# Kernel tuning notes

Hardware: AMD Instinct MI355X
Metric: run time of the kernel (lower is better)

Reference implementation:

```python
import jax, jax.numpy as jnp
import numpy as np
from jax import lax

D_MODEL = 1024
D_INNER = 2048   # expand * d_model
D_STATE = 16
DT_RANK = 128    # ceil(d_inner / 16)
K = 4            # depthwise conv kernel size
EPS = 1e-5


def setup_inputs() -> dict:
    key = jax.random.key(0)
    ks = jax.random.split(key, 12)
    x = jax.random.normal(ks[0], (2, 1024, D_MODEL), dtype=jnp.float32)
    norm_w = jnp.ones((D_MODEL,), jnp.float32)
    norm_b = jnp.zeros((D_MODEL,), jnp.float32)
    # linear weights stored (in, out)
    in_proj_w = jax.random.normal(ks[1], (D_MODEL, 2 * D_INNER), jnp.float32) * (D_MODEL ** -0.5)
    conv_w = jax.random.normal(ks[2], (D_INNER, K), jnp.float32) * (K ** -0.5)
    conv_b = jnp.zeros((D_INNER,), jnp.float32)
    x_proj_w = jax.random.normal(ks[3], (D_INNER, DT_RANK + 2 * D_STATE), jnp.float32) * (D_INNER ** -0.5)
    dt_init_std = DT_RANK ** -0.5
    dt_proj_w = jax.random.uniform(ks[4], (DT_RANK, D_INNER), jnp.float32, -dt_init_std, dt_init_std)
    dt = jnp.exp(jax.random.uniform(ks[5], (D_INNER,), jnp.float32)
                 * (np.log(0.1) - np.log(0.001)) + np.log(0.001))
    dt_proj_b = dt + jnp.log(-jnp.expm1(-dt))  # inverse-softplus init
    A_log = jax.random.normal(ks[6], (D_INNER, D_STATE), jnp.float32)
    D_param = jax.random.normal(ks[7], (D_INNER,), jnp.float32)
    out_proj_w = jax.random.normal(ks[8], (D_INNER, D_MODEL), jnp.float32) * (D_INNER ** -0.5)
    return dict(x=x, norm_w=norm_w, norm_b=norm_b, in_proj_w=in_proj_w,
                conv_w=conv_w, conv_b=conv_b, x_proj_w=x_proj_w,
                dt_proj_w=dt_proj_w, dt_proj_b=dt_proj_b, A_log=A_log,
                D_param=D_param, out_proj_w=out_proj_w)


def _layer_norm(x, w, b):
    mu = jnp.mean(x, axis=-1, keepdims=True)
    var = jnp.mean(jnp.square(x - mu), axis=-1, keepdims=True)
    return (x - mu) * lax.rsqrt(var + EPS) * w + b


def _causal_depthwise_conv(x, w, b):
    # x: (B, L, D); w: (D, K). Equivalent to torch conv1d(pad=3)[:, :, :L].
    L = x.shape[1]
    xp = jnp.pad(x, ((0, 0), (K - 1, 0), (0, 0)))
    out = b
    for k in range(K):
        out = out + w[:, k] * xp[:, k:k + L, :]
    return out


def _selective_scan(u, delta, A, B, C, D):
    # u, delta: (B, L, D); A: (D, N); B, C: (B, L, N); D: (D,)
    deltaA = jnp.exp(jnp.einsum('bld,dn->bldn', delta, A))           # (B,L,D,N)
    deltaBu = jnp.einsum('bld,bln,bld->bldn', delta, B, u)           # (B,L,D,N)
    bsz, _, d, n = deltaA.shape

    def step(h, inp):
        dA, dBu, Ct = inp
        h = dA * h + dBu                                             # (B,D,N)
        y = jnp.einsum('bdn,bn->bd', h, Ct)
        return h, y

    h0 = jnp.zeros((bsz, d, n), u.dtype)
    _, ys = lax.scan(step, h0,
                     (deltaA.transpose(1, 0, 2, 3),
                      deltaBu.transpose(1, 0, 2, 3),
                      C.transpose(1, 0, 2)))
    y = ys.transpose(1, 0, 2)                                        # (B,L,D)
    return y + u * D


def reference(x, norm_w, norm_b, in_proj_w, conv_w, conv_b, x_proj_w,
              dt_proj_w, dt_proj_b, A_log, D_param, out_proj_w):
    residual = x
    h = _layer_norm(x, norm_w, norm_b)
    xr = h @ in_proj_w                                               # (B,L,2*D_inner)
    xs, res = xr[..., :D_INNER], xr[..., D_INNER:]
    xs = _causal_depthwise_conv(xs, conv_w, conv_b)
    xs = jax.nn.silu(xs)
    # S6
    A = -jnp.exp(A_log)
    xp = xs @ x_proj_w                                               # (B,L,dt_rank+2N)
    dr = xp[..., :DT_RANK]
    Bm = xp[..., DT_RANK:DT_RANK + D_STATE]
    Cm = xp[..., DT_RANK + D_STATE:]
    delta = jax.nn.softplus(dr @ dt_proj_w + dt_proj_b)
    y = _selective_scan(xs, delta, A, Bm, Cm, D_param)
    y = y * jax.nn.silu(res)
    return y @ out_proj_w + residual
```

## Files before the change

### kernel.cpp

```cpp
#include <hip/hip_runtime.h>
#include <hip/hip_bf16.h>
#include <math.h>

#define BSZ     2
#define LLEN    1024
#define DM      1024
#define DI      2048
#define DS      16
#define DTR     128
#define NXP     160
#define MROWS   (BSZ*LLEN)
#define NCH     32
#define CHL     (LLEN/NCH)

typedef short  bf16x8 __attribute__((ext_vector_type(8)));
typedef float  f32x4  __attribute__((ext_vector_type(4)));

__device__ __forceinline__ unsigned short f2bf(float f) {
    unsigned int u = __float_as_uint(f);
    return (unsigned short)((u + 0x7FFFu + ((u >> 16) & 1u)) >> 16);
}

__global__ __launch_bounds__(256) void ln_bf16(
    const float* __restrict__ x, const float* __restrict__ w,
    const float* __restrict__ b, unsigned short* __restrict__ hb)
{
    const int r = blockIdx.x;
    const int tid = threadIdx.x;
    const float4 v = ((const float4*)(x + (size_t)r * DM))[tid];
    float s  = v.x + v.y + v.z + v.w;
    float q  = v.x*v.x + v.y*v.y + v.z*v.z + v.w*v.w;
    #pragma unroll
    for (int o = 32; o > 0; o >>= 1) {
        s += __shfl_down(s, o);
        q += __shfl_down(q, o);
    }
    __shared__ float ss[4], sq[4];
    if ((tid & 63) == 0) { ss[tid >> 6] = s; sq[tid >> 6] = q; }
    __syncthreads();
    s = ss[0] + ss[1] + ss[2] + ss[3];
    q = sq[0] + sq[1] + sq[2] + sq[3];
    const float mu  = s * (1.0f / DM);
    const float var = q * (1.0f / DM) - mu * mu;
    const float rs  = rsqrtf(var + 1e-5f);
    const float4 wv = ((const float4*)w)[tid];
    const float4 bv = ((const float4*)b)[tid];
    ushort4 ob;
    ob.x = f2bf((v.x - mu) * rs * wv.x + bv.x);
    ob.y = f2bf((v.y - mu) * rs * wv.y + bv.y);
    ob.z = f2bf((v.z - mu) * rs * wv.z + bv.z);
    ob.w = f2bf((v.w - mu) * rs * wv.w + bv.w);
    *(ushort4*)&hb[(size_t)r * DM + (tid << 2)] = ob;
}

__global__ __launch_bounds__(256) void cast_transpose3(
    const float* __restrict__ s0, unsigned short* __restrict__ d0_,
    const float* __restrict__ s1, unsigned short* __restrict__ d1_,
    const float* __restrict__ s2, unsigned short* __restrict__ d2_)
{
    const int bid = blockIdx.x;
    const float* src; unsigned short* dst; int K, N, bx, by;
    if (bid < 1024)      { src = s0; dst = d0_; K = 1024; N = 4096;
                           bx = bid & 63; by = bid >> 6; }
    else if (bid < 1120) { int lb = bid - 1024; src = s1; dst = d1_;
                           K = 2048; N = 160; bx = lb % 3; by = lb / 3; }
    else                 { int lb = bid - 1120; src = s2; dst = d2_;
                           K = 128; N = 2048; bx = lb & 31; by = lb >> 5; }
    __shared__ unsigned short t[64][68];
    const int tid = threadIdx.x;
    const int k0 = by * 64, n0 = bx * 64;
    #pragma unroll
    for (int q = 0; q < 4; ++q) {
        int idx = q * 256 + tid;
        int r = idx >> 4, c = (idx & 15) * 4;
        if (k0 + r < K) {
            #pragma unroll
            for (int e = 0; e < 4; ++e)
                if (n0 + c + e < N)
                    t[r][c + e] = f2bf(src[(size_t)(k0 + r) * N + n0 + c + e]);
        }
    }
    __syncthreads();
    #pragma unroll
    for (int q = 0; q < 4; ++q) {
        int idx = q * 256 + tid;
        int r = idx >> 4, c = (idx & 15) * 4;
        if (n0 + r < N) {
            #pragma unroll
            for (int e = 0; e < 4; ++e)
                if (k0 + c + e < K)
                    dst[(size_t)(n0 + r) * K + k0 + c + e] = t[c + e][r];
        }
    }
}

__global__ __launch_bounds__(256) void cast_transpose_g(
    const float* __restrict__ src, unsigned short* __restrict__ dst,
    int K, int N)
{
    __shared__ unsigned short t[64][68];
    const int tid = threadIdx.x;
    const int k0 = blockIdx.y * 64, n0 = blockIdx.x * 64;
    #pragma unroll
    for (int q = 0; q < 4; ++q) {
        int idx = q * 256 + tid;
        int r = idx >> 4, c = (idx & 15) * 4;
        if (k0 + r < K) {
            #pragma unroll
            for (int e = 0; e < 4; ++e)
                if (n0 + c + e < N)
                    t[r][c + e] = f2bf(src[(size_t)(k0 + r) * N + n0 + c + e]);
        }
    }
    __syncthreads();
    #pragma unroll
    for (int q = 0; q < 4; ++q) {
        int idx = q * 256 + tid;
        int r = idx >> 4, c = (idx & 15) * 4;
        if (n0 + r < N) {
            #pragma unroll
            for (int e = 0; e < 4; ++e)
                if (k0 + c + e < K)
                    dst[(size_t)(n0 + r) * K + k0 + c + e] = t[c + e][r];
        }
    }
}

template<int BM, int BN, int EPI>
__global__ __launch_bounds__(256) void gemm_bf16(
    const unsigned short* __restrict__ A,
    const unsigned short* __restrict__ Bt,
    float* __restrict__ C, int M, int N, int K, int kpb,
    const float* __restrict__ bias,
    const float* __restrict__ resid)
{
    constexpr int LDT = 72;
    __shared__ unsigned short As[BM][LDT];
    __shared__ unsigned short Bs[BN][LDT];
    const int tid  = threadIdx.x;
    const int m0   = blockIdx.y * BM;
    const int n0   = blockIdx.x * BN;
    const int kbeg = blockIdx.z * kpb;
    const int kend = kbeg + kpb;
    float* Cw = C + (size_t)blockIdx.z * M * N;
    const int wave = tid >> 6;
    const int lane = tid & 63;
    const int wr   = (wave >> 1) * (BM / 2);
    const int wc   = (wave & 1) * (BN / 2);
    constexpr int FM = BM / 32;
    constexpr int FN = BN / 32;
    const int l15 = lane & 15;
    const int kg  = lane >> 4;

    f32x4 acc[FM][FN] = {};

    for (int kt = kbeg; kt < kend; kt += 64) {
        __syncthreads();
        #pragma unroll
        for (int q = 0; q < BM / 32; ++q) {
            int idx = q * 256 + tid;
            int r = idx >> 3, c = (idx & 7) * 8;
            *(uint4*)&As[r][c] = *(const uint4*)&A[(size_t)(m0 + r) * K + kt + c];
        }
        #pragma unroll
        for (int q = 0; q < BN / 32; ++q) {
            int idx = q * 256 + tid;
            int r = idx >> 3, c = (idx & 7) * 8;
            *(uint4*)&Bs[r][c] = *(const uint4*)&Bt[(size_t)(n0 + r) * K + kt + c];
        }
        __syncthreads();
        #pragma unroll
        for (int ks = 0; ks < 2; ++ks) {
            bf16x8 af[FM], bfr[FN];
            #pragma unroll
            for (int i = 0; i < FM; ++i)
                af[i] = *(const bf16x8*)&As[wr + i * 16 + l15][ks * 32 + kg * 8];
            #pragma unroll
            for (int j = 0; j < FN; ++j)
                bfr[j] = *(const bf16x8*)&Bs[wc + j * 16 + l15][ks * 32 + kg * 8];
            #pragma unroll
            for (int i = 0; i < FM; ++i)
                #pragma unroll
                for (int j = 0; j < FN; ++j)
                    acc[i][j] = __builtin_amdgcn_mfma_f32_16x16x32_bf16(
                        af[i], bfr[j], acc[i][j], 0, 0, 0);
        }
    }
    #pragma unroll
    for (int i = 0; i < FM; ++i) {
        #pragma unroll
        for (int j = 0; j < FN; ++j) {
            const int row = m0 + wr + i * 16 + kg * 4;
            const int col = n0 + wc + j * 16 + l15;
            #pragma unroll
            for (int r = 0; r < 4; ++r) {
                float v = acc[i][j][r];
                if (EPI == 1) {
                    float t = v + bias[col];
                    v = (t > 20.f) ? t : log1pf(__expf(t));
                } else if (EPI == 2) {
                    v += resid[(size_t)(row + r) * N + col];
                }
                Cw[(size_t)(row + r) * N + col] = v;
            }
        }
    }
}

__global__ __launch_bounds__(256) void xproj_reduce(
    const float* __restrict__ P4, float* __restrict__ xp,
    unsigned short* __restrict__ drb)
{
    const int idx = blockIdx.x * 256 + threadIdx.x;
    float s = 0.f;
    #pragma unroll
    for (int j = 0; j < 4; ++j)
        s += P4[(size_t)j * (MROWS * NXP) + idx];
    xp[idx] = s;
    const int row = idx / NXP, col = idx - row * NXP;
    if (col < DTR) drb[(size_t)row * DTR + col] = f2bf(s);
}

__global__ __launch_bounds__(256) void conv_silu(
    const float* __restrict__ xr, const float* __restrict__ cw,
    const float* __restrict__ cb, float* __restrict__ xs,
    unsigned short* __restrict__ xsb, float* __restrict__ g)
{
    const int idx = blockIdx.x * 256 + threadIdx.x;
    const int d = idx & (DI - 1);
    const int t = (idx >> 11) & (LLEN - 1);
    const int b = idx >> 21;
    const float4 wv = ((const float4*)cw)[d];
    const float w[4] = {wv.x, wv.y, wv.z, wv.w};
    float acc = cb[d];
    #pragma unroll
    for (int k = 0; k < 4; ++k) {
        const int tt = t + k - 3;
        if (tt >= 0)
            acc = fmaf(w[k], xr[((size_t)(b * LLEN + tt) << 12) + d], acc);
    }
    const float sig = 1.f / (1.f + __expf(-acc));
    const float v = acc * sig;
    xs[idx] = v;
    xsb[idx] = f2bf(v);
    const float r = xr[((size_t)(b * LLEN + t) << 12) + DI + d];
    g[idx] = r / (1.f + __expf(-r));
}

__global__ __launch_bounds__(256) void scan_part(
    float* __restrict__ dio, float* __restrict__ xio,
    const float* __restrict__ xp, const float* __restrict__ A_log,
    const float* __restrict__ Dp, float* __restrict__ S)
{
    const int blk  = blockIdx.x;
    const int dgrp = blk & 15;
    const int j    = (blk >> 4) & (NCH - 1);
    const int b    = blk >> 9;
    const int c    = threadIdx.x >> 1;
    const int sg   = threadIdx.x & 1;
    const int d    = dgrp * 128 + c;
    const int nb   = sg * 8;
    float aL[8], h[8];
    #pragma unroll
    for (int n = 0; n < 8; ++n) {
        aL[n] = -__expf(A_log[d * DS + nb + n]) * 1.44269504088896f;
        h[n] = 0.f;
    }
    const float Dd = Dp[d];
    float sd = 0.f;
    const int t0 = j * CHL;
    for (int t = t0; t < t0 + CHL; ++t) {
        const size_t row = (size_t)(b * LLEN + t);
        const float dlt = dio[row * DI + d];
        const float u   = xio[row * DI + d];
        const float du  = dlt * u;
        sd += dlt;
        const float* Bp = &xp[row * NXP + DTR + nb];
        const float* Cp = &xp[row * NXP + DTR + DS + nb];
        float y = sg ? 0.f : Dd * u;
        #pragma unroll
        for (int n = 0; n < 8; ++n) {
            const float dA = exp2f(dlt * aL[n]);
            h[n] = fmaf(dA, h[n], du * Bp[n]);
            y = fmaf(h[n], Cp[n], y);
        }
        y += __shfl_xor(y, 1);
        if (!sg) {
            dio[row * DI + d] = y;
            xio[row * DI + d] = sd;
        }
    }
    float* So = &S[(((size_t)j * BSZ + b) * DI + d) * DS + nb];
    #pragma unroll
    for (int n = 0; n < 8; ++n) So[n] = h[n];
}

__global__ __launch_bounds__(256) void scan_fix(
    float* __restrict__ S, const float* __restrict__ cumD,
    const float* __restrict__ A_log)
{
    const int c = blockIdx.x * 256 + threadIdx.x;
    const int n = c & 15;
    const int d = (c >> 4) & (DI - 1);
    const int b = c >> 15;
    const float aL = -__expf(A_log[d * DS + n]) * 1.44269504088896f;
    float h = 0.f;
    #pragma unroll
    for (int j = 0; j < NCH; ++j) {
        const float sd = cumD[(size_t)(b * LLEN + j * CHL + CHL - 1) * DI + d];
        const size_t base = (((size_t)j * BSZ + b) * DI + d) * DS + n;
        const float Pj = exp2f(aL * sd);
        const float Sj = S[base];
        S[base] = h;
        h = fmaf(Pj, h, Sj);
    }
}

__global__ __launch_bounds__(256) void scan_corr(
    const float* __restrict__ yp, const float* __restrict__ cumD,
    const float* __restrict__ xp, const float* __restrict__ g,
    const float* __restrict__ A_log, const float* __restrict__ H0,
    unsigned short* __restrict__ yb)
{
    const int blk  = blockIdx.x;
    const int dgrp = blk & 15;
    const int j    = (blk >> 4) & (NCH - 1);
    const int b    = blk >> 9;
    const int c    = threadIdx.x >> 1;
    const int sg   = threadIdx.x & 1;
    const int d    = dgrp * 128 + c;
    const int nb   = sg * 8;
    float aL[8], H[8];
    const float* Hp = &H0[(((size_t)j * BSZ + b) * DI + d) * DS + nb];
    #pragma unroll
    for (int n = 0; n < 8; ++n) {
        aL[n] = -__expf(A_log[d * DS + nb + n]) * 1.44269504088896f;
        H[n] = Hp[n];
    }
    const int t0 = j * CHL;
    for (int t = t0; t < t0 + CHL; ++t) {
        const size_t row = (size_t)(b * LLEN + t);
        const float cd = cumD[row * DI + d];
        const float* Cp = &xp[row * NXP + DTR + DS + nb];
        float corr = 0.f;
        #pragma unroll
        for (int n = 0; n < 8; ++n)
            corr = fmaf(H[n] * exp2f(aL[n] * cd), Cp[n], corr);
        corr += __shfl_xor(corr, 1);
        if (!sg) {
            const float y = yp[row * DI + d] + corr;
            yb[row * DI + d] = f2bf(y * g[row * DI + d]);
        }
    }
}

extern "C" void kernel_launch(void* const* d_in, const int* in_sizes, int n_in,
                              void* d_out, int out_size, void* d_ws, size_t ws_size,
                              hipStream_t stream)
{
    (void)in_sizes; (void)n_in; (void)out_size; (void)ws_size;
    const float* x         = (const float*)d_in[0];
    const float* norm_w    = (const float*)d_in[1];
    const float* norm_b    = (const float*)d_in[2];
    const float* in_proj_w = (const float*)d_in[3];
    const float* conv_w    = (const float*)d_in[4];
    const float* conv_b    = (const float*)d_in[5];
    const float* x_proj_w  = (const float*)d_in[6];
    const float* dt_proj_w = (const float*)d_in[7];
    const float* dt_proj_b = (const float*)d_in[8];
    const float* A_log     = (const float*)d_in[9];
    const float* D_param   = (const float*)d_in[10];
    const float* out_proj_w= (const float*)d_in[11];
    float* out = (float*)d_out;

    char* ws = (char*)d_ws;
    float*          xr    = (float*)(ws);
    float*          P4    = (float*)(ws);
    float*          delta = (float*)(ws);
    float*          Sbuf  = (float*)(ws + 16777216);
    float*          xp    = (float*)(ws + 25165824);
    unsigned short* drb   = (unsigned short*)(ws + 27262976);
    float*          xs    = (float*)(ws + 33554432);
    float*          g     = (float*)(ws + 50331648);
    unsigned short* wInT  = (unsigned short*)(ws + 50331648);
    unsigned short* hb    = (unsigned short*)(ws + 58720256);
    unsigned short* wOutT = (unsigned short*)(ws + 58720256);
    unsigned short* xsb   = (unsigned short*)(ws + 67108864);
    unsigned short* yb    = (unsigned short*)(ws + 67108864);
    unsigned short* wXT   = (unsigned short*)(ws + 75497472);
    unsigned short* dtwT  = (unsigned short*)(ws + 76152832);

    ln_bf16<<<MROWS, 256, 0, stream>>>(x, norm_w, norm_b, hb);

    cast_transpose3<<<1184, 256, 0, stream>>>(
        in_proj_w, wInT, x_proj_w, wXT, dt_proj_w, dtwT);

    gemm_bf16<128, 128, 0><<<dim3(32, 16, 1), 256, 0, stream>>>(
        hb, wInT, xr, MROWS, 2 * DI, DM, DM, nullptr, nullptr);

    conv_silu<<<(BSZ * LLEN * DI) / 256, 256, 0, stream>>>(
        xr, conv_w, conv_b, xs, xsb, g);

    gemm_bf16<128, 32, 0><<<dim3(5, 16, 4), 256, 0, stream>>>(
        xsb, wXT, P4, MROWS, NXP, DI, DI / 4, nullptr, nullptr);
    xproj_reduce<<<(MROWS * NXP) / 256, 256, 0, stream>>>(P4, xp, drb);

    gemm_bf16<128, 128, 1><<<dim3(16, 16, 1), 256, 0, stream>>>(
        drb, dtwT, delta, MROWS, DI, DTR, DTR, dt_proj_b, nullptr);

    scan_part<<<BSZ * NCH * (DI / 128), 256, 0, stream>>>(
        delta, xs, xp, A_log, D_param, Sbuf);
    scan_fix<<<(BSZ * DI * DS) / 256, 256, 0, stream>>>(Sbuf, xs, A_log);
    scan_corr<<<BSZ * NCH * (DI / 128), 256, 0, stream>>>(
        delta, xs, xp, g, A_log, Sbuf, yb);

    cast_transpose_g<<<dim3(16, 32), 256, 0, stream>>>(out_proj_w, wOutT, DI, DM);

    gemm_bf16<128, 64, 2><<<dim3(16, 16, 1), 256, 0, stream>>>(
        yb, wOutT, out, MROWS, DM, DI, DI, nullptr, x);
}
```

Measured before the change: 215.0 us.

## Fuse layernorm and weight casts into one prep kernel, add 256x128 in_proj GEMM

Merges the layernorm kernel and all four weight cast-transposes, including out_proj, into one launch. The in_proj GEMM moves to a new 512-thread kernel with 256x128 tiles and register prefetch of the next K tile. The silu gate is now stored as bf16 instead of fp32, halving its write and read traffic. wOutT gets its own workspace slot so it can be produced early, and the bf16 gate adds a small rounding error in the output.

```diff
diff --git a/kernel.cpp b/kernel.cpp
--- a/kernel.cpp
+++ b/kernel.cpp
@@ -20,54 +20,60 @@
     unsigned int u = __float_as_uint(f);
     return (unsigned short)((u + 0x7FFFu + ((u >> 16) & 1u)) >> 16);
 }
-
-__global__ __launch_bounds__(256) void ln_bf16(
-    const float* __restrict__ x, const float* __restrict__ w,
-    const float* __restrict__ b, unsigned short* __restrict__ hb)
-{
-    const int r = blockIdx.x;
+__device__ __forceinline__ float bf2f(unsigned short u) {
+    return __uint_as_float((unsigned int)u << 16);
+}
+
+__global__ __launch_bounds__(256) void prep(
+    const float* __restrict__ x, const float* __restrict__ nw,
+    const float* __restrict__ nbv, unsigned short* __restrict__ hb,
+    const float* __restrict__ w0, unsigned short* __restrict__ t0,
+    const float* __restrict__ w1, unsigned short* __restrict__ t1,
+    const float* __restrict__ w2, unsigned short* __restrict__ t2,
+    const float* __restrict__ w3, unsigned short* __restrict__ t3)
+{
+    __shared__ unsigned short t[64][68];
+    __shared__ float ss[4], sq[4];
     const int tid = threadIdx.x;
-    const float4 v = ((const float4*)(x + (size_t)r * DM))[tid];
-    float s  = v.x + v.y + v.z + v.w;
-    float q  = v.x*v.x + v.y*v.y + v.z*v.z + v.w*v.w;
-    #pragma unroll
-    for (int o = 32; o > 0; o >>= 1) {
-        s += __shfl_down(s, o);
-        q += __shfl_down(q, o);
-    }
-    __shared__ float ss[4], sq[4];
-    if ((tid & 63) == 0) { ss[tid >> 6] = s; sq[tid >> 6] = q; }
-    __syncthreads();
-    s = ss[0] + ss[1] + ss[2] + ss[3];
-    q = sq[0] + sq[1] + sq[2] + sq[3];
-    const float mu  = s * (1.0f / DM);
-    const float var = q * (1.0f / DM) - mu * mu;
-    const float rs  = rsqrtf(var + 1e-5f);
-    const float4 wv = ((const float4*)w)[tid];
-    const float4 bv = ((const float4*)b)[tid];
-    ushort4 ob;
-    ob.x = f2bf((v.x - mu) * rs * wv.x + bv.x);
-    ob.y = f2bf((v.y - mu) * rs * wv.y + bv.y);
-    ob.z = f2bf((v.z - mu) * rs * wv.z + bv.z);
-    ob.w = f2bf((v.w - mu) * rs * wv.w + bv.w);
-    *(ushort4*)&hb[(size_t)r * DM + (tid << 2)] = ob;
-}
-
-__global__ __launch_bounds__(256) void cast_transpose3(
-    const float* __restrict__ s0, unsigned short* __restrict__ d0_,
-    const float* __restrict__ s1, unsigned short* __restrict__ d1_,
-    const float* __restrict__ s2, unsigned short* __restrict__ d2_)
-{
-    const int bid = blockIdx.x;
+    int bid = blockIdx.x;
+
+    if (bid < 2048) {
+        const int r = bid;
+        const float4 v = ((const float4*)(x + (size_t)r * DM))[tid];
+        float s  = v.x + v.y + v.z + v.w;
+        float q  = v.x*v.x + v.y*v.y + v.z*v.z + v.w*v.w;
+        #pragma unroll
+        for (int o = 32; o > 0; o >>= 1) {
+            s += __shfl_down(s, o);
+            q += __shfl_down(q, o);
+        }
+        if ((tid & 63) == 0) { ss[tid >> 6] = s; sq[tid >> 6] = q; }
+        __syncthreads();
+        s = ss[0] + ss[1] + ss[2] + ss[3];
+        q = sq[0] + sq[1] + sq[2] + sq[3];
+        const float mu  = s * (1.0f / DM);
+        const float var = q * (1.0f / DM) - mu * mu;
+        const float rs  = rsqrtf(var + 1e-5f);
+        const float4 wv = ((const float4*)nw)[tid];
+        const float4 bv = ((const float4*)nbv)[tid];
+        ushort4 ob;
+        ob.x = f2bf((v.x - mu) * rs * wv.x + bv.x);
+        ob.y = f2bf((v.y - mu) * rs * wv.y + bv.y);
+        ob.z = f2bf((v.z - mu) * rs * wv.z + bv.z);
+        ob.w = f2bf((v.w - mu) * rs * wv.w + bv.w);
+        *(ushort4*)&hb[(size_t)r * DM + (tid << 2)] = ob;
+        return;
+    }
+    bid -= 2048;
     const float* src; unsigned short* dst; int K, N, bx, by;
-    if (bid < 1024)      { src = s0; dst = d0_; K = 1024; N = 4096;
+    if (bid < 1024)      { src = w0; dst = t0; K = 1024; N = 4096;
                            bx = bid & 63; by = bid >> 6; }
-    else if (bid < 1120) { int lb = bid - 1024; src = s1; dst = d1_;
+    else if (bid < 1120) { int lb = bid - 1024; src = w1; dst = t1;
                            K = 2048; N = 160; bx = lb % 3; by = lb / 3; }
-    else                 { int lb = bid - 1120; src = s2; dst = d2_;
+    else if (bid < 1184) { int lb = bid - 1120; src = w2; dst = t2;
                            K = 128; N = 2048; bx = lb & 31; by = lb >> 5; }
-    __shared__ unsigned short t[64][68];
-    const int tid = threadIdx.x;
+    else                 { int lb = bid - 1184; src = w3; dst = t3;
+                           K = 2048; N = 1024; bx = lb & 15; by = lb >> 4; }
     const int k0 = by * 64, n0 = bx * 64;
     #pragma unroll
     for (int q = 0; q < 4; ++q) {
@@ -94,34 +100,89 @@
     }
 }
 
-__global__ __launch_bounds__(256) void cast_transpose_g(
-    const float* __restrict__ src, unsigned short* __restrict__ dst,
-    int K, int N)
-{
-    __shared__ unsigned short t[64][68];
-    const int tid = threadIdx.x;
-    const int k0 = blockIdx.y * 64, n0 = blockIdx.x * 64;
+__global__ __launch_bounds__(512) void gemm_big(
+    const unsigned short* __restrict__ A,
+    const unsigned short* __restrict__ Bt,
+    float* __restrict__ C, int M, int N, int K)
+{
+    constexpr int LDT = 72;
+    __shared__ unsigned short As[256][LDT];
+    __shared__ unsigned short Bs[128][LDT];
+    const int tid  = threadIdx.x;
+    const int m0   = blockIdx.y * 256;
+    const int n0   = blockIdx.x * 128;
+    const int wave = tid >> 6;
+    const int lane = tid & 63;
+    const int wr   = (wave >> 1) * 64;
+    const int wc   = (wave & 1) * 64;
+    const int l15  = lane & 15;
+    const int kg   = lane >> 4;
+
+    f32x4 acc[4][4] = {};
+
+    uint4 pA[4], pB[2];
     #pragma unroll
     for (int q = 0; q < 4; ++q) {
-        int idx = q * 256 + tid;
-        int r = idx >> 4, c = (idx & 15) * 4;
-        if (k0 + r < K) {
-            #pragma unroll
-            for (int e = 0; e < 4; ++e)
-                if (n0 + c + e < N)
-                    t[r][c + e] = f2bf(src[(size_t)(k0 + r) * N + n0 + c + e]);
-        }
-    }
-    __syncthreads();
-    #pragma unroll
-    for (int q = 0; q < 4; ++q) {
-        int idx = q * 256 + tid;
-        int r = idx >> 4, c = (idx & 15) * 4;
-        if (n0 + r < N) {
-            #pragma unroll
-            for (int e = 0; e < 4; ++e)
-                if (k0 + c + e < K)
-                    dst[(size_t)(n0 + r) * K + k0 + c + e] = t[c + e][r];
+        int idx = q * 512 + tid;
+        pA[q] = *(const uint4*)&A[(size_t)(m0 + (idx >> 3)) * K + ((idx & 7) * 8)];
+    }
+    #pragma unroll
+    for (int q = 0; q < 2; ++q) {
+        int idx = q * 512 + tid;
+        pB[q] = *(const uint4*)&Bt[(size_t)(n0 + (idx >> 3)) * K + ((idx & 7) * 8)];
+    }
+
+    for (int kt = 0; kt < K; kt += 64) {
+        __syncthreads();
+        #pragma unroll
+        for (int q = 0; q < 4; ++q) {
+            int idx = q * 512 + tid;
+            *(uint4*)&As[idx >> 3][(idx & 7) * 8] = pA[q];
+        }
+        #pragma unroll
+        for (int q = 0; q < 2; ++q) {
+            int idx = q * 512 + tid;
+            *(uint4*)&Bs[idx >> 3][(idx & 7) * 8] = pB[q];
+        }
+        if (kt + 64 < K) {
+            #pragma unroll
+            for (int q = 0; q < 4; ++q) {
+                int idx = q * 512 + tid;
+                pA[q] = *(const uint4*)&A[(size_t)(m0 + (idx >> 3)) * K + kt + 64 + ((idx & 7) * 8)];
+            }
+            #pragma unroll
+            for (int q = 0; q < 2; ++q) {
+                int idx = q * 512 + tid;
+                pB[q] = *(const uint4*)&Bt[(size_t)(n0 + (idx >> 3)) * K + kt + 64 + ((idx & 7) * 8)];
+            }
+        }
+        __syncthreads();
+        #pragma unroll
+        for (int ks = 0; ks < 2; ++ks) {
+            bf16x8 af[4], bfr[4];
+            #pragma unroll
+            for (int i = 0; i < 4; ++i)
+                af[i] = *(const bf16x8*)&As[wr + i * 16 + l15][ks * 32 + kg * 8];
+            #pragma unroll
+            for (int j = 0; j < 4; ++j)
+                bfr[j] = *(const bf16x8*)&Bs[wc + j * 16 + l15][ks * 32 + kg * 8];
+            #pragma unroll
+            for (int i = 0; i < 4; ++i)
+                #pragma unroll
+                for (int j = 0; j < 4; ++j)
+                    acc[i][j] = __builtin_amdgcn_mfma_f32_16x16x32_bf16(
+                        af[i], bfr[j], acc[i][j], 0, 0, 0);
+        }
+    }
+    #pragma unroll
+    for (int i = 0; i < 4; ++i) {
+        #pragma unroll
+        for (int j = 0; j < 4; ++j) {
+            const int row = m0 + wr + i * 16 + kg * 4;
+            const int col = n0 + wc + j * 16 + l15;
+            #pragma unroll
+            for (int r = 0; r < 4; ++r)
+                C[(size_t)(row + r) * N + col] = acc[i][j][r];
         }
     }
 }
@@ -224,7 +285,7 @@
 __global__ __launch_bounds__(256) void conv_silu(
     const float* __restrict__ xr, const float* __restrict__ cw,
     const float* __restrict__ cb, float* __restrict__ xs,
-    unsigned short* __restrict__ xsb, float* __restrict__ g)
+    unsigned short* __restrict__ xsb, unsigned short* __restrict__ gb)
 {
     const int idx = blockIdx.x * 256 + threadIdx.x;
     const int d = idx & (DI - 1);
@@ -244,7 +305,7 @@
     xs[idx] = v;
     xsb[idx] = f2bf(v);
     const float r = xr[((size_t)(b * LLEN + t) << 12) + DI + d];
-    g[idx] = r / (1.f + __expf(-r));
+    gb[idx] = f2bf(r / (1.f + __expf(-r)));
 }
 
 __global__ __launch_bounds__(256) void scan_part(
@@ -318,7 +379,7 @@
 
 __global__ __launch_bounds__(256) void scan_corr(
     const float* __restrict__ yp, const float* __restrict__ cumD,
-    const float* __restrict__ xp, const float* __restrict__ g,
+    const float* __restrict__ xp, const unsigned short* __restrict__ gb,
     const float* __restrict__ A_log, const float* __restrict__ H0,
     unsigned short* __restrict__ yb)
 {
@@ -349,7 +410,7 @@
         corr += __shfl_xor(corr, 1);
         if (!sg) {
             const float y = yp[row * DI + d] + corr;
-            yb[row * DI + d] = f2bf(y * g[row * DI + d]);
+            yb[row * DI + d] = f2bf(y * bf2f(gb[row * DI + d]));
         }
     }
 }
@@ -381,25 +442,23 @@
     float*          xp    = (float*)(ws + 25165824);
     unsigned short* drb   = (unsigned short*)(ws + 27262976);
     float*          xs    = (float*)(ws + 33554432);
-    float*          g     = (float*)(ws + 50331648);
+    unsigned short* gb    = (unsigned short*)(ws + 50331648);
     unsigned short* wInT  = (unsigned short*)(ws + 50331648);
     unsigned short* hb    = (unsigned short*)(ws + 58720256);
-    unsigned short* wOutT = (unsigned short*)(ws + 58720256);
+    unsigned short* wOutT = (unsigned short*)(ws + 62914560);
     unsigned short* xsb   = (unsigned short*)(ws + 67108864);
     unsigned short* yb    = (unsigned short*)(ws + 67108864);
     unsigned short* wXT   = (unsigned short*)(ws + 75497472);
     unsigned short* dtwT  = (unsigned short*)(ws + 76152832);
 
-    ln_bf16<<<MROWS, 256, 0, stream>>>(x, norm_w, norm_b, hb);
-
-    cast_transpose3<<<1184, 256, 0, stream>>>(
-        in_proj_w, wInT, x_proj_w, wXT, dt_proj_w, dtwT);
-
-    gemm_bf16<128, 128, 0><<<dim3(32, 16, 1), 256, 0, stream>>>(
-        hb, wInT, xr, MROWS, 2 * DI, DM, DM, nullptr, nullptr);
+    prep<<<3744, 256, 0, stream>>>(x, norm_w, norm_b, hb,
+                                   in_proj_w, wInT, x_proj_w, wXT,
+                                   dt_proj_w, dtwT, out_proj_w, wOutT);
+
+    gemm_big<<<dim3(32, 8), 512, 0, stream>>>(hb, wInT, xr, MROWS, 2 * DI, DM);
 
     conv_silu<<<(BSZ * LLEN * DI) / 256, 256, 0, stream>>>(
-        xr, conv_w, conv_b, xs, xsb, g);
+        xr, conv_w, conv_b, xs, xsb, gb);
 
     gemm_bf16<128, 32, 0><<<dim3(5, 16, 4), 256, 0, stream>>>(
         xsb, wXT, P4, MROWS, NXP, DI, DI / 4, nullptr, nullptr);
@@ -412,9 +471,7 @@
         delta, xs, xp, A_log, D_param, Sbuf);
     scan_fix<<<(BSZ * DI * DS) / 256, 256, 0, stream>>>(Sbuf, xs, A_log);
     scan_corr<<<BSZ * NCH * (DI / 128), 256, 0, stream>>>(
-        delta, xs, xp, g, A_log, Sbuf, yb);
-
-    cast_transpose_g<<<dim3(16, 32), 256, 0, stream>>>(out_proj_w, wOutT, DI, DM);
+        delta, xs, xp, gb, A_log, Sbuf, yb);
 
     gemm_bf16<128, 64, 2><<<dim3(16, 16, 1), 256, 0, stream>>>(
         yb, wOutT, out, MROWS, DM, DI, DI, nullptr, x);
```

Result: slower. 255.2 us (+18.7%).
